# Kernel optimization log

Measured on AMD Instinct MI355X. Metric: run time of the kernel, lower is better.

Reference implementation:

```python
import jax, jax.numpy as jnp
import numpy as np


def setup_inputs() -> dict:
    key = jax.random.key(0)
    k1, k2, k3, k4, k5 = jax.random.split(key, 5)
    B, T, U, D, H, V = 4, 256, 96, 512, 512, 1024
    return {
        "encoder_outputs": jax.random.normal(k1, (B, T, D), dtype=jnp.float32),
        "decoder_outputs": jax.random.normal(k2, (B, U, D), dtype=jnp.float32),
        # W1: torch Linear(input_size=2D -> H) weight, stored here as (2D, H)
        "W1": jax.random.normal(k3, (2 * D, H), dtype=jnp.float32) * 0.02,
        "b1": jax.random.normal(k4, (H,), dtype=jnp.float32) * 0.02,
        # W2: torch Linear(H -> V, bias=False) weight, stored as (H, V)
        "W2": jax.random.normal(k5, (H, V), dtype=jnp.float32) * 0.02,
    }


def reference(encoder_outputs, decoder_outputs, W1, b1, W2):
    # Faithful to: repeat/cat to (B,T,U,2D) -> Linear -> GELU(tanh) -> Linear.
    # concat-then-Linear == split W1 into enc/dec halves and broadcast-add,
    # which avoids materializing the (B,T,U,2D) tensor (same math exactly).
    D = encoder_outputs.shape[-1]
    We, Wd = W1[:D], W1[D:]                      # (D,H), (D,H)
    he = jnp.einsum("btd,dh->bth", encoder_outputs, We)   # (B,T,H)
    hd = jnp.einsum("bud,dh->buh", decoder_outputs, Wd)   # (B,U,H)
    h = he[:, :, None, :] + hd[:, None, :, :] + b1         # (B,T,U,H)
    h = jax.nn.gelu(h, approximate=True)                   # tanh GELU
    return jnp.einsum("btuh,hv->btuv", h, W2)              # (B,T,U,V)
```

## Files before the change

kernel.cpp:

```cpp
#include <hip/hip_runtime.h>
#include <hip/hip_bf16.h>

typedef __attribute__((ext_vector_type(8))) short short8;
typedef __attribute__((ext_vector_type(4))) float f32x4;

__device__ __forceinline__ unsigned short f2bf(float f) {
    union { __hip_bfloat16 h; unsigned short u; } cv;
    cv.h = __float2bfloat16(f);
    return cv.u;
}

__device__ __forceinline__ float gelu_t(float x) {
    float e = __expf(1.5957691216057308f * x * __builtin_fmaf(0.044715f, x * x, 1.0f));
    return x * (e / (e + 1.0f));
}

__device__ __forceinline__ void gload_lds16(const void* g, void* l) {
    __builtin_amdgcn_global_load_lds((const __attribute__((address_space(1))) unsigned int*)g,
                                     (__attribute__((address_space(3))) unsigned int*)l, 16, 0, 0);
}

__device__ __forceinline__ int swzkey(int r) { return ((r >> 1) & 3) << 4; }

__global__ __launch_bounds__(256) void transpose_all(const float* __restrict__ W1,
                                                     const float* __restrict__ W2,
                                                     unsigned short* __restrict__ Wet,
                                                     unsigned short* __restrict__ Wdt,
                                                     unsigned short* __restrict__ W2t) {
    int z = blockIdx.z;
    if (z < 2 && blockIdx.y >= 8) return;
    const float* in = (z == 0) ? W1 : (z == 1) ? (W1 + 512 * 512) : W2;
    unsigned short* out = (z == 0) ? Wet : (z == 1) ? Wdt : W2t;
    int N = (z == 2) ? 1024 : 512;

    __shared__ float tile[64][65];
    int k0 = blockIdx.x * 64, n0 = blockIdx.y * 64;
    int t = threadIdx.x;
    int c = t & 63, r0 = t >> 6;
#pragma unroll
    for (int i = 0; i < 16; i++) {
        int r = r0 + i * 4;
        tile[r][c] = in[(size_t)(k0 + r) * N + n0 + c];
    }
    __syncthreads();
    int kk = t & 15;
    int nl0 = t >> 4;
#pragma unroll
    for (int i = 0; i < 4; i++) {
        int nl = nl0 + i * 16;
        int n  = n0 + nl;
        unsigned short b0 = f2bf(tile[kk * 4 + 0][nl]);
        unsigned short b1 = f2bf(tile[kk * 4 + 1][nl]);
        unsigned short b2 = f2bf(tile[kk * 4 + 2][nl]);
        unsigned short b3 = f2bf(tile[kk * 4 + 3][nl]);
        uint2 v;
        v.x = (unsigned)b0 | ((unsigned)b1 << 16);
        v.y = (unsigned)b2 | ((unsigned)b3 << 16);
        int byte_in_chunk = kk * 8;
        int slice = byte_in_chunk & ~63;
        int off   = (byte_in_chunk & 63) ^ swzkey(n);
        size_t obyte = (size_t)n * 1024 + (size_t)k0 * 2 + slice + off;
        *(uint2*)((char*)out + obyte) = v;
    }
}

__global__ __launch_bounds__(256, 2) void gemm_small(const float* __restrict__ enc,
                                                     const float* __restrict__ dec,
                                                     const unsigned short* __restrict__ Wet,
                                                     const unsigned short* __restrict__ Wdt,
                                                     const float* __restrict__ b1,
                                                     float* __restrict__ he,
                                                     float* __restrict__ hd) {
    bool isEnc = blockIdx.x < 8;
    const float* A = isEnc ? enc : dec;
    const unsigned short* Bt = isEnc ? Wet : Wdt;
    const float* bias = isEnc ? b1 : nullptr;
    float* C = isEnc ? he : hd;
    size_t m0 = (size_t)(isEnc ? blockIdx.x : blockIdx.x - 8) * 128;

    __shared__ alignas(16) unsigned short As[128 * 32];
    __shared__ alignas(16) unsigned short Bs[128 * 32];
    int t = threadIdx.x;
    int n0 = blockIdx.y * 128;
    int lane = t & 63, w = t >> 6;
    int wm = w >> 1, wn = w & 1;
    int rA = t >> 3, cg = t & 7;
    f32x4 acc[4][4] = {};

    for (int kt = 0; kt < 16; ++kt) {
        int k0 = kt * 32;
        __syncthreads();
#pragma unroll
        for (int p = 0; p < 4; p++) {
            int r = rA + p * 32;
            f32x4 v = *(const f32x4*)&A[(m0 + r) * 512 + k0 + cg * 4];
            uint2 pk;
            pk.x = (unsigned)f2bf(v.x) | ((unsigned)f2bf(v.y) << 16);
            pk.y = (unsigned)f2bf(v.z) | ((unsigned)f2bf(v.w) << 16);
            int off = (cg * 8) ^ swzkey(r);
            *(uint2*)((char*)As + r * 64 + off) = pk;
        }
#pragma unroll
        for (int j = 0; j < 2; j++) {
            int ibyte = w * 1024 + j * 4096;
            int lb = ibyte + lane * 16;
            int row = lb >> 6, colb = lb & 63;
            const char* src = (const char*)Bt + (size_t)(n0 + row) * 1024 + k0 * 2 + colb;
            gload_lds16(src, (char*)Bs + ibyte);
        }
        __syncthreads();
        short8 af[4], bf[4];
#pragma unroll
        for (int mi = 0; mi < 4; mi++) {
            int r = wm * 64 + mi * 16 + (lane & 15);
            int off = ((lane >> 4) * 16) ^ swzkey(r);
            af[mi] = *(const short8*)((const char*)As + r * 64 + off);
        }
#pragma unroll
        for (int ni = 0; ni < 4; ni++) {
            int n = wn * 64 + ni * 16 + (lane & 15);
            int off = ((lane >> 4) * 16) ^ swzkey(n);
            bf[ni] = *(const short8*)((const char*)Bs + n * 64 + off);
        }
#pragma unroll
        for (int mi = 0; mi < 4; mi++)
#pragma unroll
            for (int ni = 0; ni < 4; ni++)
                acc[mi][ni] = __builtin_amdgcn_mfma_f32_16x16x32_bf16(af[mi], bf[ni], acc[mi][ni], 0, 0, 0);
    }
#pragma unroll
    for (int mi = 0; mi < 4; mi++) {
        int row = wm * 64 + mi * 16 + ((lane >> 4) << 2);
#pragma unroll
        for (int ni = 0; ni < 4; ni++) {
            int col = n0 + wn * 64 + ni * 16 + (lane & 15);
            float bv = bias ? bias[col] : 0.0f;
#pragma unroll
            for (int q = 0; q < 4; q++)
                C[(m0 + row + q) * 512 + col] = acc[mi][ni][q] + bv;
        }
    }
}

__global__ __launch_bounds__(512, 4) void joint_fused(const float* __restrict__ he,
                                                      const float* __restrict__ hd,
                                                      const unsigned short* __restrict__ W2t,
                                                      float* __restrict__ out) {
    __shared__ alignas(16) char lds[73728];
    int t = threadIdx.x;
    int lane = t & 63, w = t >> 6;
    int bx = blockIdx.x;
    int mt = (bx & 7) * 192 + (bx >> 3);
    size_t m0 = (size_t)mt * 64;
    int n0 = blockIdx.y * 512;

    int rA = t >> 3, cg = t & 7;
    int mrow = (int)m0 + rA;
    int tI = mrow / 96;
    int u  = mrow - tI * 96;
    const float* eP = he + (size_t)tI * 512 + cg * 4;
    const float* dP = hd + (size_t)((tI >> 8) * 96 + u) * 512 + cg * 4;
    int aoff = rA * 64 + ((cg * 8) ^ swzkey(rA));

    const char* bSrc[4];
#pragma unroll
    for (int i = 0; i < 4; i++) {
        int row = w * 64 + i * 16 + (lane >> 2);
        bSrc[i] = (const char*)W2t + (size_t)(n0 + row) * 1024 + (lane & 3) * 16;
    }

    int l15 = lane & 15, lg = lane >> 4;
    int aOff[4], bOff[4];
#pragma unroll
    for (int mi = 0; mi < 4; mi++) {
        int r = mi * 16 + l15;
        aOff[mi] = r * 64 + ((lg * 16) ^ swzkey(r));
    }
#pragma unroll
    for (int ni = 0; ni < 4; ni++) {
        int n = w * 64 + ni * 16 + l15;
        bOff[ni] = 8192 + n * 64 + ((lg * 16) ^ swzkey(n));
    }

    f32x4 acc[4][4] = {};
    f32x4 er[2], dr[2];

#define LOADED(slot, kt)  do { \
        er[slot] = *(const f32x4*)(eP + (kt) * 32); \
        dr[slot] = *(const f32x4*)(dP + (kt) * 32); } while (0)

#define STAGE_B(buf, kt)  do { \
        _Pragma("unroll") \
        for (int i = 0; i < 4; i++) \
            gload_lds16(bSrc[i] + (kt) * 64, lds + 8192 + (buf) * 32768 + w * 4096 + i * 1024); } while (0)

#define GELU_A(buf, slot) do { \
        uint2 pk; \
        pk.x = (unsigned)f2bf(gelu_t(er[slot].x + dr[slot].x)) | \
               ((unsigned)f2bf(gelu_t(er[slot].y + dr[slot].y)) << 16); \
        pk.y = (unsigned)f2bf(gelu_t(er[slot].z + dr[slot].z)) | \
               ((unsigned)f2bf(gelu_t(er[slot].w + dr[slot].w)) << 16); \
        *(uint2*)(lds + (buf) * 4096 + aoff) = pk; } while (0)

    STAGE_B(0, 0);
    LOADED(0, 0);
    LOADED(1, 1);
    GELU_A(0, 0);
    asm volatile("s_waitcnt lgkmcnt(0)" ::: "memory");
    asm volatile("s_waitcnt vmcnt(2)" ::: "memory");
    __builtin_amdgcn_sched_barrier(0);
    __builtin_amdgcn_s_barrier();
    __builtin_amdgcn_sched_barrier(0);

#pragma unroll
    for (int kt = 0; kt < 16; ++kt) {
        const int cur = kt & 1, nxt = cur ^ 1;
        if (kt < 15) STAGE_B(nxt, kt + 1);
        if (kt < 14) LOADED(cur, kt + 2);
        if (kt < 15) GELU_A(nxt, nxt);
        short8 a[4];
#pragma unroll
        for (int mi = 0; mi < 4; mi++) a[mi] = *(const short8*)(lds + cur * 4096 + aOff[mi]);
        __builtin_amdgcn_s_setprio(1);
#pragma unroll
        for (int ni = 0; ni < 4; ni++) {
            short8 b = *(const short8*)(lds + cur * 32768 + bOff[ni]);
#pragma unroll
            for (int mi = 0; mi < 4; mi++)
                acc[mi][ni] = __builtin_amdgcn_mfma_f32_16x16x32_bf16(a[mi], b, acc[mi][ni], 0, 0, 0);
        }
        __builtin_amdgcn_s_setprio(0);
        if (kt < 15) {
            asm volatile("s_waitcnt lgkmcnt(0)" ::: "memory");
            __builtin_amdgcn_sched_barrier(0);
            if (kt < 14) asm volatile("s_waitcnt vmcnt(2)" ::: "memory");
            else         asm volatile("s_waitcnt vmcnt(0)" ::: "memory");
            __builtin_amdgcn_sched_barrier(0);
            __builtin_amdgcn_s_barrier();
            __builtin_amdgcn_sched_barrier(0);
        }
    }
#undef LOADED
#undef STAGE_B
#undef GELU_A

    asm volatile("s_waitcnt lgkmcnt(0)" ::: "memory");
    __builtin_amdgcn_sched_barrier(0);
    __builtin_amdgcn_s_barrier();
    __builtin_amdgcn_sched_barrier(0);

    char* ep = lds + w * 4864;
#pragma unroll
    for (int mi = 0; mi < 4; mi++) {
#pragma unroll
        for (int ni = 0; ni < 4; ni++)
#pragma unroll
            for (int q = 0; q < 4; q++)
                *(float*)(ep + (lg * 4 + q) * 304 + (ni * 16 + l15) * 4) = acc[mi][ni][q];
        asm volatile("s_waitcnt lgkmcnt(0)" ::: "memory");
        __builtin_amdgcn_sched_barrier(0);
#pragma unroll
        for (int it = 0; it < 4; it++) {
            int r = it * 4 + lg;
            f32x4 v = *(const f32x4*)(ep + r * 304 + l15 * 16);
            size_t row = m0 + mi * 16 + r;
            float* o = out + row * 1024 + n0 + w * 64 + l15 * 4;
            __builtin_nontemporal_store(v, (f32x4*)o);
        }
        asm volatile("s_waitcnt lgkmcnt(0)" ::: "memory");
        __builtin_amdgcn_sched_barrier(0);
    }
}

extern "C" void kernel_launch(void* const* d_in, const int* in_sizes, int n_in,
                              void* d_out, int out_size, void* d_ws, size_t ws_size,
                              hipStream_t stream) {
    const float* enc = (const float*)d_in[0];
    const float* dec = (const float*)d_in[1];
    const float* W1  = (const float*)d_in[2];
    const float* b1  = (const float*)d_in[3];
    const float* W2  = (const float*)d_in[4];
    float* out = (float*)d_out;

    char* ws = (char*)d_ws;
    float* he = (float*)(ws);
    float* hd = (float*)(ws + 2097152);
    unsigned short* Wet = (unsigned short*)(ws + 2883584);
    unsigned short* Wdt = (unsigned short*)(ws + 3407872);
    unsigned short* W2t = (unsigned short*)(ws + 3932160);

    transpose_all<<<dim3(8, 16, 3), 256, 0, stream>>>(W1, W2, Wet, Wdt, W2t);
    gemm_small<<<dim3(11, 4), 256, 0, stream>>>(enc, dec, Wet, Wdt, b1, he, hd);
    joint_fused<<<dim3(1536, 2), 512, 0, stream>>>(he, hd, W2t, out);
}
```

Baseline: 191.2 us.

## Overlap W2 transpose with smaller-tile he/hd GEMM in one prep kernel

```diff
diff --git a/kernel.cpp b/kernel.cpp
--- a/kernel.cpp
+++ b/kernel.cpp
@@ -22,16 +22,13 @@
 
 __device__ __forceinline__ int swzkey(int r) { return ((r >> 1) & 3) << 4; }
 
-__global__ __launch_bounds__(256) void transpose_all(const float* __restrict__ W1,
-                                                     const float* __restrict__ W2,
-                                                     unsigned short* __restrict__ Wet,
-                                                     unsigned short* __restrict__ Wdt,
-                                                     unsigned short* __restrict__ W2t) {
+__global__ __launch_bounds__(256) void transpose_wewd(const float* __restrict__ W1,
+                                                      unsigned short* __restrict__ Wet,
+                                                      unsigned short* __restrict__ Wdt) {
     int z = blockIdx.z;
-    if (z < 2 && blockIdx.y >= 8) return;
-    const float* in = (z == 0) ? W1 : (z == 1) ? (W1 + 512 * 512) : W2;
-    unsigned short* out = (z == 0) ? Wet : (z == 1) ? Wdt : W2t;
-    int N = (z == 2) ? 1024 : 512;
+    const float* in = (z == 0) ? W1 : (W1 + 512 * 512);
+    unsigned short* out = (z == 0) ? Wet : Wdt;
+    const int N = 512;
 
     __shared__ float tile[64][65];
     int k0 = blockIdx.x * 64, n0 = blockIdx.y * 64;
@@ -64,34 +61,74 @@
     }
 }
 
-__global__ __launch_bounds__(256, 2) void gemm_small(const float* __restrict__ enc,
-                                                     const float* __restrict__ dec,
-                                                     const unsigned short* __restrict__ Wet,
-                                                     const unsigned short* __restrict__ Wdt,
-                                                     const float* __restrict__ b1,
-                                                     float* __restrict__ he,
-                                                     float* __restrict__ hd) {
-    bool isEnc = blockIdx.x < 8;
+__global__ __launch_bounds__(256) void prep2(const float* __restrict__ enc,
+                                             const float* __restrict__ dec,
+                                             const float* __restrict__ W2,
+                                             const unsigned short* __restrict__ Wet,
+                                             const unsigned short* __restrict__ Wdt,
+                                             const float* __restrict__ b1,
+                                             unsigned short* __restrict__ W2t,
+                                             float* __restrict__ he,
+                                             float* __restrict__ hd) {
+    __shared__ alignas(16) char pbuf[16640];
+    int t = threadIdx.x;
+    int bx = blockIdx.x;
+
+    if (bx < 128) {
+        float (*tile)[65] = (float(*)[65])pbuf;
+        int k0 = (bx & 7) * 64, n0 = (bx >> 3) * 64;
+        int c = t & 63, r0 = t >> 6;
+#pragma unroll
+        for (int i = 0; i < 16; i++) {
+            int r = r0 + i * 4;
+            tile[r][c] = W2[(size_t)(k0 + r) * 1024 + n0 + c];
+        }
+        __syncthreads();
+        int kk = t & 15;
+        int nl0 = t >> 4;
+#pragma unroll
+        for (int i = 0; i < 4; i++) {
+            int nl = nl0 + i * 16;
+            int n  = n0 + nl;
+            unsigned short b0 = f2bf(tile[kk * 4 + 0][nl]);
+            unsigned short b1 = f2bf(tile[kk * 4 + 1][nl]);
+            unsigned short b2 = f2bf(tile[kk * 4 + 2][nl]);
+            unsigned short b3 = f2bf(tile[kk * 4 + 3][nl]);
+            uint2 v;
+            v.x = (unsigned)b0 | ((unsigned)b1 << 16);
+            v.y = (unsigned)b2 | ((unsigned)b3 << 16);
+            int byte_in_chunk = kk * 8;
+            int slice = byte_in_chunk & ~63;
+            int off   = (byte_in_chunk & 63) ^ swzkey(n);
+            size_t obyte = (size_t)n * 1024 + (size_t)k0 * 2 + slice + off;
+            *(uint2*)((char*)W2t + obyte) = v;
+        }
+        return;
+    }
+
+    int id  = bx - 128;
+    int ny  = id & 7;
+    int mid = id >> 3;
+    bool isEnc = mid < 16;
     const float* A = isEnc ? enc : dec;
     const unsigned short* Bt = isEnc ? Wet : Wdt;
     const float* bias = isEnc ? b1 : nullptr;
     float* C = isEnc ? he : hd;
-    size_t m0 = (size_t)(isEnc ? blockIdx.x : blockIdx.x - 8) * 128;
-
-    __shared__ alignas(16) unsigned short As[128 * 32];
-    __shared__ alignas(16) unsigned short Bs[128 * 32];
-    int t = threadIdx.x;
-    int n0 = blockIdx.y * 128;
+    size_t m0 = (size_t)(isEnc ? mid : mid - 16) * 64;
+    int n0 = ny * 64;
+
+    unsigned short* As = (unsigned short*)pbuf;
+    unsigned short* Bs = (unsigned short*)(pbuf + 4096);
     int lane = t & 63, w = t >> 6;
     int wm = w >> 1, wn = w & 1;
     int rA = t >> 3, cg = t & 7;
-    f32x4 acc[4][4] = {};
+    f32x4 acc[2][2] = {};
 
     for (int kt = 0; kt < 16; ++kt) {
         int k0 = kt * 32;
         __syncthreads();
 #pragma unroll
-        for (int p = 0; p < 4; p++) {
+        for (int p = 0; p < 2; p++) {
             int r = rA + p * 32;
             f32x4 v = *(const f32x4*)&A[(m0 + r) * 512 + k0 + cg * 4];
             uint2 pk;
@@ -100,40 +137,39 @@
             int off = (cg * 8) ^ swzkey(r);
             *(uint2*)((char*)As + r * 64 + off) = pk;
         }
-#pragma unroll
-        for (int j = 0; j < 2; j++) {
-            int ibyte = w * 1024 + j * 4096;
+        {
+            int ibyte = w * 1024;
             int lb = ibyte + lane * 16;
             int row = lb >> 6, colb = lb & 63;
             const char* src = (const char*)Bt + (size_t)(n0 + row) * 1024 + k0 * 2 + colb;
             gload_lds16(src, (char*)Bs + ibyte);
         }
         __syncthreads();
-        short8 af[4], bf[4];
-#pragma unroll
-        for (int mi = 0; mi < 4; mi++) {
-            int r = wm * 64 + mi * 16 + (lane & 15);
+        short8 af[2], bf[2];
+#pragma unroll
+        for (int mi = 0; mi < 2; mi++) {
+            int r = wm * 32 + mi * 16 + (lane & 15);
             int off = ((lane >> 4) * 16) ^ swzkey(r);
             af[mi] = *(const short8*)((const char*)As + r * 64 + off);
         }
 #pragma unroll
-        for (int ni = 0; ni < 4; ni++) {
-            int n = wn * 64 + ni * 16 + (lane & 15);
+        for (int ni = 0; ni < 2; ni++) {
+            int n = wn * 32 + ni * 16 + (lane & 15);
             int off = ((lane >> 4) * 16) ^ swzkey(n);
             bf[ni] = *(const short8*)((const char*)Bs + n * 64 + off);
         }
 #pragma unroll
-        for (int mi = 0; mi < 4; mi++)
-#pragma unroll
-            for (int ni = 0; ni < 4; ni++)
+        for (int mi = 0; mi < 2; mi++)
+#pragma unroll
+            for (int ni = 0; ni < 2; ni++)
                 acc[mi][ni] = __builtin_amdgcn_mfma_f32_16x16x32_bf16(af[mi], bf[ni], acc[mi][ni], 0, 0, 0);
     }
 #pragma unroll
-    for (int mi = 0; mi < 4; mi++) {
-        int row = wm * 64 + mi * 16 + ((lane >> 4) << 2);
-#pragma unroll
-        for (int ni = 0; ni < 4; ni++) {
-            int col = n0 + wn * 64 + ni * 16 + (lane & 15);
+    for (int mi = 0; mi < 2; mi++) {
+        int row = wm * 32 + mi * 16 + ((lane >> 4) << 2);
+#pragma unroll
+        for (int ni = 0; ni < 2; ni++) {
+            int col = n0 + wn * 32 + ni * 16 + (lane & 15);
             float bv = bias ? bias[col] : 0.0f;
 #pragma unroll
             for (int q = 0; q < 4; q++)
@@ -221,7 +257,6 @@
         short8 a[4];
 #pragma unroll
         for (int mi = 0; mi < 4; mi++) a[mi] = *(const short8*)(lds + cur * 4096 + aOff[mi]);
-        __builtin_amdgcn_s_setprio(1);
 #pragma unroll
         for (int ni = 0; ni < 4; ni++) {
             short8 b = *(const short8*)(lds + cur * 32768 + bOff[ni]);
@@ -229,7 +264,6 @@
             for (int mi = 0; mi < 4; mi++)
                 acc[mi][ni] = __builtin_amdgcn_mfma_f32_16x16x32_bf16(a[mi], b, acc[mi][ni], 0, 0, 0);
         }
-        __builtin_amdgcn_s_setprio(0);
         if (kt < 15) {
             asm volatile("s_waitcnt lgkmcnt(0)" ::: "memory");
             __builtin_amdgcn_sched_barrier(0);
@@ -289,7 +323,7 @@
     unsigned short* Wdt = (unsigned short*)(ws + 3407872);
     unsigned short* W2t = (unsigned short*)(ws + 3932160);
 
-    transpose_all<<<dim3(8, 16, 3), 256, 0, stream>>>(W1, W2, Wet, Wdt, W2t);
-    gemm_small<<<dim3(11, 4), 256, 0, stream>>>(enc, dec, Wet, Wdt, b1, he, hd);
+    transpose_wewd<<<dim3(8, 8, 2), 256, 0, stream>>>(W1, Wet, Wdt);
+    prep2<<<304, 256, 0, stream>>>(enc, dec, W2, Wet, Wdt, b1, W2t, he, hd);
     joint_fused<<<dim3(1536, 2), 512, 0, stream>>>(he, hd, W2t, out);
 }
```

Result: no change. 193.3 us (+1.1%).
